# Kernel tuning notes

Measured on AMD Instinct MI355X. Metric: run time of the kernel, lower is better.

Reference implementation:

```python
import jax, jax.numpy as jnp
import numpy as np

P = 2048       # output dim (genes)
D = 64         # latent dim
H1, H2 = 512, 512  # n_neurons
E = 16         # num_experts
N = 2048       # batch
GATE_H = 64    # gate hidden width


def _glorot(key, shape):
    fan_in, fan_out = shape[-2], shape[-1]
    lim = jnp.sqrt(6.0 / (fan_in + fan_out)).astype(jnp.float32)
    return jax.random.uniform(key, shape, jnp.float32, -lim, lim)


def setup_inputs() -> dict:
    key = jax.random.key(0)
    ks = jax.random.split(key, 12)
    z = jax.random.normal(ks[0], (N, D), jnp.float32)
    # stacked per-expert MLP weights: d -> H1 -> H2 -> p
    W1 = _glorot(ks[1], (E, D, H1));  b1 = jnp.zeros((E, H1), jnp.float32)
    W2 = _glorot(ks[2], (E, H1, H2)); b2 = jnp.zeros((E, H2), jnp.float32)
    W3 = _glorot(ks[3], (E, H2, P));  b3 = jnp.zeros((E, P), jnp.float32)
    # gate network: d -> 64 -> E
    Wg1 = _glorot(ks[4], (D, GATE_H)); bg1 = jnp.zeros((GATE_H,), jnp.float32)
    Wg2 = _glorot(ks[5], (GATE_H, E)); bg2 = jnp.zeros((E,), jnp.float32)
    # expert assignment matrix A: [p, E], binary; ensure no all-zero row
    u = jax.random.uniform(ks[6], (P, E))
    A = jnp.where(u < 0.5, 1.0, 0.0).astype(jnp.float32)
    A = A.at[:, 0].set(1.0)
    return {"z": z, "W1": W1, "b1": b1, "W2": W2, "b2": b2,
            "W3": W3, "b3": b3, "Wg1": Wg1, "bg1": bg1,
            "Wg2": Wg2, "bg2": bg2, "A": A}


def reference(z, W1, b1, W2, b2, W3, b3, Wg1, bg1, Wg2, bg2, A):
    # experts, batched across E (replaces Python loop over nn.ModuleList)
    h = jax.nn.relu(jnp.einsum('nd,edh->neh', z, W1) + b1[None])      # [N,E,H1]
    h = jax.nn.relu(jnp.einsum('neh,ehk->nek', h, W2) + b2[None])     # [N,E,H2]
    expert_out = jnp.einsum('nek,ekp->nep', h, W3) + b3[None]         # [N,E,P]
    # gate network + softmax over experts
    g = jax.nn.relu(z @ Wg1 + bg1) @ Wg2 + bg2                        # [N,E]
    gate = jax.nn.softmax(g, axis=1)                                  # [N,E]
    # feature-wise gating: gate[n,e] * A[p,e], normalized over experts
    fw = gate[:, None, :] * A[None, :, :]                             # [N,P,E]
    fw = fw / (jnp.sum(fw, axis=2, keepdims=True) + 1e-8)
    # weighted combine: sum_e expert_out[n,e,p] * fw[n,p,e]
    x_rec = jnp.einsum('nep,npe->np', expert_out, fw)                 # [N,P]
    return (x_rec, fw)
```

## Files before the change

kernel.cpp:

```cpp
#include <hip/hip_runtime.h>
#include <hip/hip_bf16.h>

#define NN   2048
#define DD   64
#define HH1  512
#define HH2  512
#define PP   2048
#define EE   16
#define KBIG (EE * HH2)
#define SPLITS 2

typedef unsigned short ushort_t;
typedef __attribute__((ext_vector_type(8))) short bf16x8;
typedef __attribute__((ext_vector_type(4))) float f32x4;

__device__ __forceinline__ float b2f(ushort_t u) {
  union { unsigned int i; float f; } v; v.i = ((unsigned int)u) << 16; return v.f;
}
__device__ __forceinline__ ushort_t f2b(float f) {
  union { float f; unsigned int i; } v; v.f = f;
  unsigned int x = v.i;
  unsigned int r = (x + 0x7fffu + ((x >> 16) & 1u)) >> 16;
  return (ushort_t)r;
}
__device__ __forceinline__ float ldf(const void* p, size_t i, int isb) {
  return isb ? b2f(((const ushort_t*)p)[i]) : ((const float*)p)[i];
}

__device__ __forceinline__ void async16(ushort_t* lds, const ushort_t* g) {
  __builtin_amdgcn_global_load_lds(
      (const __attribute__((address_space(1))) void*)g,
      (__attribute__((address_space(3))) void*)lds, 16, 0, 0);
}

__global__ void k_sniff(const unsigned int* __restrict__ zraw,
                        int* __restrict__ flag) {
  __shared__ int cnt[256];
  int t = threadIdx.x;
  int c = 0;
  for (int i = t; i < 1024; i += 256) {
    unsigned int u = zraw[i];
    unsigned int e = (u >> 7) & 0xFFu;
    c += (e >= 110u && e <= 135u) ? 1 : 0;
  }
  cnt[t] = c;
  __syncthreads();
  for (int s = 128; s > 0; s >>= 1) {
    if (t < s) cnt[t] += cnt[t + s];
    __syncthreads();
  }
  if (t == 0) *flag = (cnt[0] >= 512) ? 1 : 0;
}

__global__ void k_probe(int* __restrict__ mapflag) {
  __shared__ ushort_t Ap[16 * 32];
  __shared__ ushort_t Bp[16 * 32];
  int t = threadIdx.x;
  for (int i = t; i < 512; i += 64) {
    int r = i >> 5, k = i & 31;
    Ap[i] = f2b((float)((r + k) % 7));
    Bp[i] = f2b((float)((2 * r + k) % 5));
  }
  __syncthreads();
  int lr = t & 15, quad = t >> 4;
  bf16x8 a = *(const bf16x8*)&Ap[lr * 32 + quad * 8];
  bf16x8 b = *(const bf16x8*)&Bp[lr * 32 + quad * 8];
  f32x4 acc = {};
  acc = __builtin_amdgcn_mfma_f32_16x16x32_bf16(a, b, acc, 0, 0, 0);
  bool m0 = true, m1 = true;
  for (int r = 0; r < 4; ++r) {
    float r0 = 0.f, r1 = 0.f;
    for (int k = 0; k < 32; ++k) {
      r0 += (float)(((quad * 4 + r) + k) % 7) * (float)((2 * lr + k) % 5);
      r1 += (float)((lr + k) % 7) * (float)((2 * (quad * 4 + r) + k) % 5);
    }
    m0 &= fabsf(acc[r] - r0) < 0.5f;
    m1 &= fabsf(acc[r] - r1) < 0.5f;
  }
  unsigned long long b0 = __ballot(m0);
  unsigned long long b1 = __ballot(m1);
  if (t == 0) *mapflag = (b0 == ~0ULL) ? 0 : ((b1 == ~0ULL) ? 1 : 0);
}

__global__ void k_convert(const void* __restrict__ src,
                          ushort_t* __restrict__ dst, int n,
                          const int* __restrict__ flag) {
  int isb = *flag;
  int stride = gridDim.x * blockDim.x;
  for (int g = blockIdx.x * blockDim.x + threadIdx.x; g * 8 < n; g += stride) {
    int base = g * 8;
    ushort_t ov[8];
    if (isb) {
      *(uint4*)ov = *(const uint4*)((const ushort_t*)src + base);
    } else {
      const float* s = (const float*)src + base;
      float4 f0 = *(const float4*)s;
      float4 f1 = *(const float4*)(s + 4);
      ov[0] = f2b(f0.x); ov[1] = f2b(f0.y); ov[2] = f2b(f0.z); ov[3] = f2b(f0.w);
      ov[4] = f2b(f1.x); ov[5] = f2b(f1.y); ov[6] = f2b(f1.z); ov[7] = f2b(f1.w);
    }
    *(uint4*)(dst + base) = *(uint4*)ov;
  }
}

__global__ void k_transpose_cvt(const void* __restrict__ src_,
                                ushort_t* __restrict__ dst, int K, int H,
                                int ld_dst, long e_dst_off,
                                const void* __restrict__ Amask,
                                const int* __restrict__ flag) {
  __shared__ ushort_t tile[64][68];
  int isb = *flag;
  int e = blockIdx.z;
  size_t ebase = (size_t)e * K * H;
  dst += (size_t)e * e_dst_off;
  int h0 = blockIdx.x * 64, k0 = blockIdx.y * 64;
  int t = threadIdx.x;
#pragma unroll
  for (int it = 0; it < 2; ++it) {
    int c = it * 256 + t;
    int row = c >> 3, col = (c & 7) * 8;
    size_t idx = ebase + (size_t)(k0 + row) * H + h0 + col;
    ushort_t tmp[8];
    if (isb) {
      *(uint4*)tmp = *(const uint4*)((const ushort_t*)src_ + idx);
    } else {
      const float* s = (const float*)src_ + idx;
      float4 f0 = *(const float4*)s;
      float4 f1 = *(const float4*)(s + 4);
      tmp[0] = f2b(f0.x); tmp[1] = f2b(f0.y); tmp[2] = f2b(f0.z); tmp[3] = f2b(f0.w);
      tmp[4] = f2b(f1.x); tmp[5] = f2b(f1.y); tmp[6] = f2b(f1.z); tmp[7] = f2b(f1.w);
    }
#pragma unroll
    for (int j = 0; j < 8; ++j) tile[row][col + j] = tmp[j];
  }
  __syncthreads();
#pragma unroll
  for (int it = 0; it < 2; ++it) {
    int c = it * 256 + t;
    int row = c >> 3, col = (c & 7) * 8;
    ushort_t tmp[8];
#pragma unroll
    for (int j = 0; j < 8; ++j) tmp[j] = tile[col + j][row];
    if (Amask) {
      float a = ldf(Amask, (size_t)(h0 + row) * EE + e, isb);
#pragma unroll
      for (int j = 0; j < 8; ++j) tmp[j] = f2b(a * b2f(tmp[j]));
    }
    *(uint4*)(dst + (size_t)(h0 + row) * ld_dst + k0 + col) = *(uint4*)tmp;
  }
}

__global__ void k_gate(const void* __restrict__ z,
                       const void* __restrict__ Wg1,
                       const void* __restrict__ bg1,
                       const void* __restrict__ Wg2,
                       const void* __restrict__ bg2,
                       const int* __restrict__ flag,
                       float* __restrict__ gate) {
  __shared__ float sW1[64][65];
  __shared__ float sW2[64][16];
  __shared__ float sb1[64];
  __shared__ float sb2[16];
  __shared__ float sz[4][64];
  __shared__ float shid[4][64];
  __shared__ float sg[4][16];
  int isb = *flag;
  int t = threadIdx.x;
  for (int i = t; i < 64 * 64; i += 256) sW1[i >> 6][i & 63] = ldf(Wg1, i, isb);
  for (int i = t; i < 64 * 16; i += 256) sW2[i >> 4][i & 15] = ldf(Wg2, i, isb);
  if (t < 64) sb1[t] = ldf(bg1, t, isb);
  if (t < 16) sb2[t] = ldf(bg2, t, isb);
  int w = t >> 6, l = t & 63;
  int n = blockIdx.x * 4 + w;
  sz[w][l] = ldf(z, (size_t)n * DD + l, isb);
  __syncthreads();
  float acc = sb1[l];
#pragma unroll
  for (int d = 0; d < 64; ++d) acc += sz[w][d] * sW1[d][l];
  shid[w][l] = fmaxf(acc, 0.f);
  __syncthreads();
  if (l < 16) {
    float g = sb2[l];
#pragma unroll
    for (int j = 0; j < 64; ++j) g += shid[w][j] * sW2[j][l];
    sg[w][l] = g;
  }
  __syncthreads();
  if (l < 16) {
    float m = -1e30f;
    for (int e2 = 0; e2 < 16; ++e2) m = fmaxf(m, sg[w][e2]);
    float s = 0.f;
    for (int e2 = 0; e2 < 16; ++e2) s += __expf(sg[w][e2] - m);
    gate[(size_t)n * EE + l] = __expf(sg[w][l] - m) / s;
  }
}

__global__ __launch_bounds__(256) void k_gemm_bt_relu(
    const ushort_t* __restrict__ Aact, const ushort_t* __restrict__ Bt,
    const ushort_t* __restrict__ bias, ushort_t* __restrict__ Cout,
    int M, int K, int ldc,
    long a_stride_e, long b_stride_e, long bias_stride_e, long c_stride_e,
    const float* __restrict__ gs,
    const int* __restrict__ mapflag) {
  __shared__ ushort_t As[128 * 32];
  __shared__ ushort_t Bs[128 * 32];
  int e = blockIdx.z;
  Aact += (size_t)e * a_stride_e;
  Bt   += (size_t)e * b_stride_e;
  bias += (size_t)e * bias_stride_e;
  Cout += (size_t)e * c_stride_e;
  int m0 = blockIdx.y * 128, n0 = blockIdx.x * 128;
  int t = threadIdx.x;
  int w = t >> 6, l = t & 63;
  int wm = (w >> 1) * 64, wn = (w & 1) * 64;
  int lr = l & 15, quad = l >> 4;
  int mf = *mapflag;

  f32x4 acc[4][4] = {};
  for (int k0 = 0; k0 < K; k0 += 32) {
#pragma unroll
    for (int it = 0; it < 2; ++it) {
      int c = it * 256 + t;
      int row = c >> 2, kk = (c & 3) * 8;
      async16(&As[row * 32 + kk], Aact + (size_t)(m0 + row) * K + k0 + kk);
    }
#pragma unroll
    for (int it = 0; it < 2; ++it) {
      int c = it * 256 + t;
      int row = c >> 2, kk = (c & 3) * 8;
      async16(&Bs[row * 32 + kk], Bt + (size_t)(n0 + row) * K + k0 + kk);
    }
    __syncthreads();
    bf16x8 af[4], bfr[4];
#pragma unroll
    for (int i = 0; i < 4; ++i)
      af[i] = *(const bf16x8*)&As[(wm + i * 16 + lr) * 32 + quad * 8];
#pragma unroll
    for (int j = 0; j < 4; ++j)
      bfr[j] = *(const bf16x8*)&Bs[(wn + j * 16 + lr) * 32 + quad * 8];
#pragma unroll
    for (int i = 0; i < 4; ++i)
#pragma unroll
      for (int j = 0; j < 4; ++j)
        acc[i][j] = __builtin_amdgcn_mfma_f32_16x16x32_bf16(af[i], bfr[j],
                                                            acc[i][j], 0, 0, 0);
    __syncthreads();
  }
  if (mf == 0) {
    float gv[4][4];
#pragma unroll
    for (int i = 0; i < 4; ++i)
#pragma unroll
      for (int r = 0; r < 4; ++r)
        gv[i][r] = gs ? gs[(size_t)(m0 + wm + i * 16 + quad * 4 + r) * EE + e]
                      : 1.f;
#pragma unroll
    for (int j = 0; j < 4; ++j) {
      int n = n0 + wn + j * 16 + lr;
      float bv = b2f(bias[n]);
#pragma unroll
      for (int i = 0; i < 4; ++i)
#pragma unroll
        for (int r = 0; r < 4; ++r) {
          int m = m0 + wm + i * 16 + quad * 4 + r;
          Cout[(size_t)m * ldc + n] =
              f2b(fmaxf(acc[i][j][r] + bv, 0.f) * gv[i][r]);
        }
    }
  } else {
#pragma unroll
    for (int i = 0; i < 4; ++i) {
      int m = m0 + wm + i * 16 + lr;
      float gvi = gs ? gs[(size_t)m * EE + e] : 1.f;
#pragma unroll
      for (int j = 0; j < 4; ++j)
#pragma unroll
        for (int r = 0; r < 4; ++r) {
          int n = n0 + wn + j * 16 + quad * 4 + r;
          Cout[(size_t)m * ldc + n] =
              f2b(fmaxf(acc[i][j][r] + b2f(bias[n]), 0.f) * gvi);
        }
    }
  }
}

__global__ __launch_bounds__(256) void k_bigk(
    const ushort_t* __restrict__ Ab,
    const ushort_t* __restrict__ Bb,
    float* __restrict__ part,
    const int* __restrict__ mapflag) {
  __shared__ ushort_t As[128 * 32];
  __shared__ ushort_t Bs[128 * 32];
  int s = blockIdx.z;
  int m0 = blockIdx.y * 128, n0 = blockIdx.x * 128;
  int t = threadIdx.x;
  int w = t >> 6, l = t & 63;
  int wm = (w >> 1) * 64, wn = (w & 1) * 64;
  int lr = l & 15, quad = l >> 4;
  int mf = *mapflag;
  float* out = part + (size_t)s * NN * PP;
  int kbeg = s * (KBIG / SPLITS), kend = kbeg + KBIG / SPLITS;

  f32x4 acc[4][4] = {};
  for (int k0 = kbeg; k0 < kend; k0 += 32) {
#pragma unroll
    for (int it = 0; it < 2; ++it) {
      int c = it * 256 + t;
      int row = c >> 2, kk = (c & 3) * 8;
      async16(&As[row * 32 + kk], Ab + (size_t)(m0 + row) * KBIG + k0 + kk);
    }
#pragma unroll
    for (int it = 0; it < 2; ++it) {
      int c = it * 256 + t;
      int row = c >> 2, kk = (c & 3) * 8;
      async16(&Bs[row * 32 + kk], Bb + (size_t)(n0 + row) * KBIG + k0 + kk);
    }
    __syncthreads();
    bf16x8 af[4], bfr[4];
#pragma unroll
    for (int i = 0; i < 4; ++i)
      af[i] = *(const bf16x8*)&As[(wm + i * 16 + lr) * 32 + quad * 8];
#pragma unroll
    for (int j = 0; j < 4; ++j)
      bfr[j] = *(const bf16x8*)&Bs[(wn + j * 16 + lr) * 32 + quad * 8];
#pragma unroll
    for (int i = 0; i < 4; ++i)
#pragma unroll
      for (int j = 0; j < 4; ++j)
        acc[i][j] = __builtin_amdgcn_mfma_f32_16x16x32_bf16(af[i], bfr[j],
                                                            acc[i][j], 0, 0, 0);
    __syncthreads();
  }
  if (mf == 0) {
#pragma unroll
    for (int j = 0; j < 4; ++j) {
      int n = n0 + wn + j * 16 + lr;
#pragma unroll
      for (int i = 0; i < 4; ++i)
#pragma unroll
        for (int r = 0; r < 4; ++r) {
          int m = m0 + wm + i * 16 + quad * 4 + r;
          out[(size_t)m * PP + n] = acc[i][j][r];
        }
    }
  } else {
#pragma unroll
    for (int i = 0; i < 4; ++i) {
      int m = m0 + wm + i * 16 + lr;
#pragma unroll
      for (int j = 0; j < 4; ++j)
#pragma unroll
        for (int r = 0; r < 4; ++r) {
          int n = n0 + wn + j * 16 + quad * 4 + r;
          out[(size_t)m * PP + n] = acc[i][j][r];
        }
    }
  }
}

__global__ void k_fw_final(const float* __restrict__ gate,
                           const ushort_t* __restrict__ Amat,
                           const ushort_t* __restrict__ b3,
                           const float* __restrict__ part,
                           float* __restrict__ xrec,
                           float* __restrict__ fw) {
  __shared__ float sg[16];
  int n = blockIdx.y;
  int p = blockIdx.x * 256 + threadIdx.x;
  if (threadIdx.x < 16) sg[threadIdx.x] = gate[(size_t)n * EE + threadIdx.x];
  __syncthreads();
  uint4 a0 = *(const uint4*)(Amat + (size_t)p * EE);
  uint4 a1 = *(const uint4*)(Amat + (size_t)p * EE + 8);
  ushort_t av[16];
  *(uint4*)av = a0;
  *(uint4*)(av + 8) = a1;
  float wv[16];
  float s = 0.f, bias = 0.f;
#pragma unroll
  for (int e = 0; e < 16; ++e) {
    wv[e] = sg[e] * b2f(av[e]);
    s += wv[e];
    bias += wv[e] * b2f(b3[(size_t)e * PP + p]);
  }
  float inv = 1.f / (s + 1e-8f);
  size_t np = (size_t)n * PP + p;
  float num = part[np] + part[(size_t)NN * PP + np] + bias;
  xrec[np] = num * inv;
  float* dst = fw + np * EE;
#pragma unroll
  for (int e = 0; e < 16; ++e) wv[e] *= inv;
  *(float4*)(dst + 0)  = *(float4*)(wv + 0);
  *(float4*)(dst + 4)  = *(float4*)(wv + 4);
  *(float4*)(dst + 8)  = *(float4*)(wv + 8);
  *(float4*)(dst + 12) = *(float4*)(wv + 12);
}

extern "C" void kernel_launch(void* const* d_in, const int* in_sizes, int n_in,
                              void* d_out, int out_size, void* d_ws,
                              size_t ws_size, hipStream_t stream) {
  const void* z_r   = d_in[0];
  const void* W1_r  = d_in[1];
  const void* b1_r  = d_in[2];
  const void* W2_r  = d_in[3];
  const void* b2_r  = d_in[4];
  const void* W3_r  = d_in[5];
  const void* b3_r  = d_in[6];
  const void* Wg1_r = d_in[7];
  const void* bg1_r = d_in[8];
  const void* Wg2_r = d_in[9];
  const void* bg2_r = d_in[10];
  const void* A_r   = d_in[11];

  float* xrec = (float*)d_out;
  float* fw   = (float*)d_out + (size_t)NN * PP;

  char* ws = (char*)d_ws;
  int* flag    = (int*)ws;             ws += 128;
  int* mapflag = (int*)ws;             ws += 128;
  float* gate = (float*)ws;            ws += (size_t)NN * EE * 4;
  ushort_t* zC   = (ushort_t*)ws;      ws += (size_t)NN * DD * 2;
  ushort_t* b1C  = (ushort_t*)ws;      ws += (size_t)EE * HH1 * 2;
  ushort_t* b2C  = (ushort_t*)ws;      ws += (size_t)EE * HH2 * 2;
  ushort_t* b3C  = (ushort_t*)ws;      ws += (size_t)EE * PP * 2;
  ushort_t* AC   = (ushort_t*)ws;      ws += (size_t)PP * EE * 2;
  ushort_t* W1t = (ushort_t*)ws;       ws += (size_t)EE * HH1 * DD * 2;
  ushort_t* W2t = (ushort_t*)ws;       ws += (size_t)EE * HH2 * HH1 * 2;
  ushort_t* W3big = (ushort_t*)ws;     ws += (size_t)PP * KBIG * 2;
  ushort_t* H2big = (ushort_t*)ws;     ws += (size_t)NN * KBIG * 2;
  ushort_t* h1  = (ushort_t*)ws;       ws += (size_t)EE * NN * HH1 * 2;
  float* partial = (float*)h1;

  k_sniff<<<1, 256, 0, stream>>>((const unsigned int*)z_r, flag);
  k_probe<<<1, 64, 0, stream>>>(mapflag);

  auto cvt = [&](const void* src, ushort_t* dst, int n) {
    int blocks = (n / 8 + 255) / 256;
    if (blocks < 1) blocks = 1;
    k_convert<<<blocks, 256, 0, stream>>>(src, dst, n, flag);
  };
  cvt(z_r,  zC,  NN * DD);
  cvt(b1_r, b1C, EE * HH1);
  cvt(b2_r, b2C, EE * HH2);
  cvt(b3_r, b3C, EE * PP);
  cvt(A_r,  AC,  PP * EE);

  k_transpose_cvt<<<dim3(HH1 / 64, DD / 64, EE), 256, 0, stream>>>(
      W1_r, W1t, DD, HH1, DD, (long)HH1 * DD, nullptr, flag);
  k_transpose_cvt<<<dim3(HH2 / 64, HH1 / 64, EE), 256, 0, stream>>>(
      W2_r, W2t, HH1, HH2, HH1, (long)HH2 * HH1, nullptr, flag);
  k_transpose_cvt<<<dim3(PP / 64, HH2 / 64, EE), 256, 0, stream>>>(
      W3_r, W3big, HH2, PP, KBIG, (long)HH2, A_r, flag);

  k_gate<<<NN / 4, 256, 0, stream>>>(z_r, Wg1_r, bg1_r, Wg2_r, bg2_r, flag, gate);

  k_gemm_bt_relu<<<dim3(HH1 / 128, NN / 128, EE), 256, 0, stream>>>(
      zC, W1t, b1C, h1, NN, DD, HH1,
      0, (long)HH1 * DD, HH1, (long)NN * HH1, nullptr, mapflag);
  k_gemm_bt_relu<<<dim3(HH2 / 128, NN / 128, EE), 256, 0, stream>>>(
      h1, W2t, b2C, H2big, NN, HH1, KBIG,
      (long)NN * HH1, (long)HH2 * HH1, HH2, (long)HH2, gate, mapflag);

  k_bigk<<<dim3(PP / 128, NN / 128, SPLITS), 256, 0, stream>>>(
      H2big, W3big, partial, mapflag);

  k_fw_final<<<dim3(PP / 256, NN), 256, 0, stream>>>(
      gate, AC, b3C, partial, xrec, fw);
}
```

Measured before the change: 600.3 us.

## Double-buffer GEMM LDS tiles, swizzle blocks across XCDs, adaptive split-K

```diff
diff --git a/kernel.cpp b/kernel.cpp
--- a/kernel.cpp
+++ b/kernel.cpp
@@ -8,7 +8,6 @@
 #define PP   2048
 #define EE   16
 #define KBIG (EE * HH2)
-#define SPLITS 2
 
 typedef unsigned short ushort_t;
 typedef __attribute__((ext_vector_type(8))) short bf16x8;
@@ -31,6 +30,12 @@
   __builtin_amdgcn_global_load_lds(
       (const __attribute__((address_space(1))) void*)g,
       (__attribute__((address_space(3))) void*)lds, 16, 0, 0);
+}
+
+__device__ __forceinline__ int xcd_swz(int orig, int nwg) {
+  int q = nwg >> 3, r = nwg & 7;
+  int xcd = orig & 7, loc = orig >> 3;
+  return (xcd < r ? xcd * (q + 1) : r * (q + 1) + (xcd - r) * q) + loc;
 }
 
 __global__ void k_sniff(const unsigned int* __restrict__ zraw,
@@ -202,14 +207,16 @@
     long a_stride_e, long b_stride_e, long bias_stride_e, long c_stride_e,
     const float* __restrict__ gs,
     const int* __restrict__ mapflag) {
-  __shared__ ushort_t As[128 * 32];
-  __shared__ ushort_t Bs[128 * 32];
+  __shared__ ushort_t As[2][128 * 32];
+  __shared__ ushort_t Bs[2][128 * 32];
   int e = blockIdx.z;
   Aact += (size_t)e * a_stride_e;
   Bt   += (size_t)e * b_stride_e;
   bias += (size_t)e * bias_stride_e;
   Cout += (size_t)e * c_stride_e;
-  int m0 = blockIdx.y * 128, n0 = blockIdx.x * 128;
+  int nxy = gridDim.x * gridDim.y;
+  int swz = xcd_swz(blockIdx.x + gridDim.x * blockIdx.y, nxy);
+  int m0 = (swz / gridDim.x) * 128, n0 = (swz % gridDim.x) * 128;
   int t = threadIdx.x;
   int w = t >> 6, l = t & 63;
   int wm = (w >> 1) * 64, wn = (w & 1) * 64;
@@ -217,27 +224,35 @@
   int mf = *mapflag;
 
   f32x4 acc[4][4] = {};
+#pragma unroll
+  for (int it = 0; it < 2; ++it) {
+    int c = it * 256 + t;
+    int row = c >> 2, kk = (c & 3) * 8;
+    async16(&As[0][row * 32 + kk], Aact + (size_t)(m0 + row) * K + kk);
+    async16(&Bs[0][row * 32 + kk], Bt + (size_t)(n0 + row) * K + kk);
+  }
+  __syncthreads();
+  int cur = 0;
   for (int k0 = 0; k0 < K; k0 += 32) {
-#pragma unroll
-    for (int it = 0; it < 2; ++it) {
-      int c = it * 256 + t;
-      int row = c >> 2, kk = (c & 3) * 8;
-      async16(&As[row * 32 + kk], Aact + (size_t)(m0 + row) * K + k0 + kk);
-    }
-#pragma unroll
-    for (int it = 0; it < 2; ++it) {
-      int c = it * 256 + t;
-      int row = c >> 2, kk = (c & 3) * 8;
-      async16(&Bs[row * 32 + kk], Bt + (size_t)(n0 + row) * K + k0 + kk);
-    }
-    __syncthreads();
+    if (k0 + 32 < K) {
+      int nxt = cur ^ 1;
+#pragma unroll
+      for (int it = 0; it < 2; ++it) {
+        int c = it * 256 + t;
+        int row = c >> 2, kk = (c & 3) * 8;
+        async16(&As[nxt][row * 32 + kk],
+                Aact + (size_t)(m0 + row) * K + k0 + 32 + kk);
+        async16(&Bs[nxt][row * 32 + kk],
+                Bt + (size_t)(n0 + row) * K + k0 + 32 + kk);
+      }
+    }
     bf16x8 af[4], bfr[4];
 #pragma unroll
     for (int i = 0; i < 4; ++i)
-      af[i] = *(const bf16x8*)&As[(wm + i * 16 + lr) * 32 + quad * 8];
+      af[i] = *(const bf16x8*)&As[cur][(wm + i * 16 + lr) * 32 + quad * 8];
 #pragma unroll
     for (int j = 0; j < 4; ++j)
-      bfr[j] = *(const bf16x8*)&Bs[(wn + j * 16 + lr) * 32 + quad * 8];
+      bfr[j] = *(const bf16x8*)&Bs[cur][(wn + j * 16 + lr) * 32 + quad * 8];
 #pragma unroll
     for (int i = 0; i < 4; ++i)
 #pragma unroll
@@ -245,6 +260,7 @@
         acc[i][j] = __builtin_amdgcn_mfma_f32_16x16x32_bf16(af[i], bfr[j],
                                                             acc[i][j], 0, 0, 0);
     __syncthreads();
+    cur ^= 1;
   }
   if (mf == 0) {
     float gv[4][4];
@@ -288,41 +304,53 @@
     const ushort_t* __restrict__ Ab,
     const ushort_t* __restrict__ Bb,
     float* __restrict__ part,
+    int splits,
     const int* __restrict__ mapflag) {
-  __shared__ ushort_t As[128 * 32];
-  __shared__ ushort_t Bs[128 * 32];
+  __shared__ ushort_t As[2][128 * 32];
+  __shared__ ushort_t Bs[2][128 * 32];
   int s = blockIdx.z;
-  int m0 = blockIdx.y * 128, n0 = blockIdx.x * 128;
+  int nxy = gridDim.x * gridDim.y;
+  int swz = xcd_swz(blockIdx.x + gridDim.x * blockIdx.y, nxy);
+  int m0 = (swz / gridDim.x) * 128, n0 = (swz % gridDim.x) * 128;
   int t = threadIdx.x;
   int w = t >> 6, l = t & 63;
   int wm = (w >> 1) * 64, wn = (w & 1) * 64;
   int lr = l & 15, quad = l >> 4;
   int mf = *mapflag;
   float* out = part + (size_t)s * NN * PP;
-  int kbeg = s * (KBIG / SPLITS), kend = kbeg + KBIG / SPLITS;
+  int kspan = KBIG / splits;
+  int kbeg = s * kspan, kend = kbeg + kspan;
 
   f32x4 acc[4][4] = {};
+#pragma unroll
+  for (int it = 0; it < 2; ++it) {
+    int c = it * 256 + t;
+    int row = c >> 2, kk = (c & 3) * 8;
+    async16(&As[0][row * 32 + kk], Ab + (size_t)(m0 + row) * KBIG + kbeg + kk);
+    async16(&Bs[0][row * 32 + kk], Bb + (size_t)(n0 + row) * KBIG + kbeg + kk);
+  }
+  __syncthreads();
+  int cur = 0;
   for (int k0 = kbeg; k0 < kend; k0 += 32) {
-#pragma unroll
-    for (int it = 0; it < 2; ++it) {
-      int c = it * 256 + t;
-      int row = c >> 2, kk = (c & 3) * 8;
-      async16(&As[row * 32 + kk], Ab + (size_t)(m0 + row) * KBIG + k0 + kk);
-    }
-#pragma unroll
-    for (int it = 0; it < 2; ++it) {
-      int c = it * 256 + t;
-      int row = c >> 2, kk = (c & 3) * 8;
-      async16(&Bs[row * 32 + kk], Bb + (size_t)(n0 + row) * KBIG + k0 + kk);
-    }
-    __syncthreads();
+    if (k0 + 32 < kend) {
+      int nxt = cur ^ 1;
+#pragma unroll
+      for (int it = 0; it < 2; ++it) {
+        int c = it * 256 + t;
+        int row = c >> 2, kk = (c & 3) * 8;
+        async16(&As[nxt][row * 32 + kk],
+                Ab + (size_t)(m0 + row) * KBIG + k0 + 32 + kk);
+        async16(&Bs[nxt][row * 32 + kk],
+                Bb + (size_t)(n0 + row) * KBIG + k0 + 32 + kk);
+      }
+    }
     bf16x8 af[4], bfr[4];
 #pragma unroll
     for (int i = 0; i < 4; ++i)
-      af[i] = *(const bf16x8*)&As[(wm + i * 16 + lr) * 32 + quad * 8];
+      af[i] = *(const bf16x8*)&As[cur][(wm + i * 16 + lr) * 32 + quad * 8];
 #pragma unroll
     for (int j = 0; j < 4; ++j)
-      bfr[j] = *(const bf16x8*)&Bs[(wn + j * 16 + lr) * 32 + quad * 8];
+      bfr[j] = *(const bf16x8*)&Bs[cur][(wn + j * 16 + lr) * 32 + quad * 8];
 #pragma unroll
     for (int i = 0; i < 4; ++i)
 #pragma unroll
@@ -330,6 +358,7 @@
         acc[i][j] = __builtin_amdgcn_mfma_f32_16x16x32_bf16(af[i], bfr[j],
                                                             acc[i][j], 0, 0, 0);
     __syncthreads();
+    cur ^= 1;
   }
   if (mf == 0) {
 #pragma unroll
@@ -358,41 +387,44 @@
   }
 }
 
-__global__ void k_fw_final(const float* __restrict__ gate,
-                           const ushort_t* __restrict__ Amat,
-                           const ushort_t* __restrict__ b3,
-                           const float* __restrict__ part,
-                           float* __restrict__ xrec,
-                           float* __restrict__ fw) {
-  __shared__ float sg[16];
-  int n = blockIdx.y;
-  int p = blockIdx.x * 256 + threadIdx.x;
-  if (threadIdx.x < 16) sg[threadIdx.x] = gate[(size_t)n * EE + threadIdx.x];
-  __syncthreads();
-  uint4 a0 = *(const uint4*)(Amat + (size_t)p * EE);
-  uint4 a1 = *(const uint4*)(Amat + (size_t)p * EE + 8);
-  ushort_t av[16];
-  *(uint4*)av = a0;
-  *(uint4*)(av + 8) = a1;
-  float wv[16];
-  float s = 0.f, bias = 0.f;
-#pragma unroll
-  for (int e = 0; e < 16; ++e) {
-    wv[e] = sg[e] * b2f(av[e]);
-    s += wv[e];
-    bias += wv[e] * b2f(b3[(size_t)e * PP + p]);
-  }
-  float inv = 1.f / (s + 1e-8f);
-  size_t np = (size_t)n * PP + p;
-  float num = part[np] + part[(size_t)NN * PP + np] + bias;
-  xrec[np] = num * inv;
-  float* dst = fw + np * EE;
-#pragma unroll
-  for (int e = 0; e < 16; ++e) wv[e] *= inv;
-  *(float4*)(dst + 0)  = *(float4*)(wv + 0);
-  *(float4*)(dst + 4)  = *(float4*)(wv + 4);
-  *(float4*)(dst + 8)  = *(float4*)(wv + 8);
-  *(float4*)(dst + 12) = *(float4*)(wv + 12);
+__global__ __launch_bounds__(256) void k_fw_final(
+    const float* __restrict__ gate,
+    const ushort_t* __restrict__ Amat,
+    const ushort_t* __restrict__ b3,
+    const float* __restrict__ part,
+    int splits,
+    float* __restrict__ xrec,
+    float* __restrict__ fw) {
+  size_t stride = (size_t)gridDim.x * blockDim.x;
+  for (size_t i = (size_t)blockIdx.x * blockDim.x + threadIdx.x;
+       i < (size_t)NN * PP; i += stride) {
+    int n = (int)(i >> 11);
+    int p = (int)(i & (PP - 1));
+    uint4 a0 = *(const uint4*)(Amat + (size_t)p * EE);
+    uint4 a1 = *(const uint4*)(Amat + (size_t)p * EE + 8);
+    ushort_t av[16];
+    *(uint4*)av = a0;
+    *(uint4*)(av + 8) = a1;
+    float wv[16];
+    float s = 0.f, bias = 0.f;
+#pragma unroll
+    for (int e = 0; e < 16; ++e) {
+      wv[e] = gate[(size_t)n * EE + e] * b2f(av[e]);
+      s += wv[e];
+      bias += wv[e] * b2f(b3[(size_t)e * PP + p]);
+    }
+    float num = bias;
+    for (int sp = 0; sp < splits; ++sp) num += part[(size_t)sp * NN * PP + i];
+    float inv = 1.f / (s + 1e-8f);
+    xrec[i] = num * inv;
+    float* dst = fw + i * EE;
+#pragma unroll
+    for (int e = 0; e < 16; ++e) wv[e] *= inv;
+    *(float4*)(dst + 0)  = *(float4*)(wv + 0);
+    *(float4*)(dst + 4)  = *(float4*)(wv + 4);
+    *(float4*)(dst + 8)  = *(float4*)(wv + 8);
+    *(float4*)(dst + 12) = *(float4*)(wv + 12);
+  }
 }
 
 extern "C" void kernel_launch(void* const* d_in, const int* in_sizes, int n_in,
@@ -429,6 +461,8 @@
   ushort_t* H2big = (ushort_t*)ws;     ws += (size_t)NN * KBIG * 2;
   ushort_t* h1  = (ushort_t*)ws;       ws += (size_t)EE * NN * HH1 * 2;
   float* partial = (float*)h1;
+  size_t off_h1 = (size_t)((char*)h1 - (char*)d_ws);
+  int splits = (ws_size >= off_h1 + (size_t)4 * NN * PP * 4) ? 4 : 2;
 
   k_sniff<<<1, 256, 0, stream>>>((const unsigned int*)z_r, flag);
   k_probe<<<1, 64, 0, stream>>>(mapflag);
@@ -460,9 +494,9 @@
       h1, W2t, b2C, H2big, NN, HH1, KBIG,
       (long)NN * HH1, (long)HH2 * HH1, HH2, (long)HH2, gate, mapflag);
 
-  k_bigk<<<dim3(PP / 128, NN / 128, SPLITS), 256, 0, stream>>>(
-      H2big, W3big, partial, mapflag);
-
-  k_fw_final<<<dim3(PP / 256, NN), 256, 0, stream>>>(
-      gate, AC, b3C, partial, xrec, fw);
-}
+  k_bigk<<<dim3(PP / 128, NN / 128, splits), 256, 0, stream>>>(
+      H2big, W3big, partial, splits, mapflag);
+
+  k_fw_final<<<2048, 256, 0, stream>>>(
+      gate, AC, b3C, partial, splits, xrec, fw);
+}
```

After: 610.2 us. About the same (+1.6%).
